# Optimization experiments

Hardware: AMD Instinct MI355X
Metric: run time of the kernel (lower is better)

Reference implementation:

```python
import jax, jax.numpy as jnp
import numpy as np

DECAY = 0.99
EPS = 1e-5
BETA = 0.25

def _l2norm(v, axis=-1):
    # F.normalize: x / max(||x||, 1e-12)
    n = jnp.sqrt(jnp.sum(v * v, axis=axis, keepdims=True))
    return v / jnp.maximum(n, 1e-12)

def setup_inputs() -> dict:
    key = jax.random.key(0)
    k0, k1, k2, k3 = jax.random.split(key, 4)
    B, C, H, W, E, K = 8, 256, 64, 64, 32, 8192
    x = jax.random.normal(k0, (B, C, H, W), jnp.float32)
    Wq = jax.random.normal(k1, (E, C), jnp.float32) * 0.05  # 1x1 conv kernel
    bq = jnp.zeros((E,), jnp.float32)
    emb = jax.random.normal(k2, (K, E), jnp.float32)
    emb = _l2norm(emb, axis=1)  # matches F.normalize init in __init__
    ema_cluster_size = jnp.ones((K,), jnp.float32)
    ema_weight = emb  # consistent post-init EMA state
    return {"x": x, "Wq": Wq, "bq": bq, "embedding": emb,
            "ema_cluster_size": ema_cluster_size, "ema_weight": ema_weight}

def reference(x, Wq, bq, embedding, ema_cluster_size, ema_weight):
    B, C, H, W = x.shape
    E = Wq.shape[0]
    K = embedding.shape[0]
    # quant_conv: 1x1 conv == per-pixel linear
    z = jnp.einsum('bchw,ec->behw', x, Wq) + bq[None, :, None, None]  # [B,E,H,W]
    z_flat = z.transpose(0, 2, 3, 1).reshape(-1, E)  # [N,E]
    # get_idx(use_znorm=True): cosine similarity argmax (== argmin L2 on normalized)
    zn = _l2norm(z_flat, axis=1)
    en = _l2norm(embedding, axis=1)
    indices = jnp.argmax(zn @ en.T, axis=1)  # [N]
    # codebook gather (raw embedding, as in torch)
    z_q = embedding[indices].reshape(B, H, W, E).transpose(0, 3, 1, 2)  # [B,E,H,W]
    # EMA update (training path; scatter == one-hot.T @ z_flat / one-hot.sum)
    counts = jax.ops.segment_sum(jnp.ones((z_flat.shape[0],), z_flat.dtype), indices, num_segments=K)
    dw = jax.ops.segment_sum(z_flat, indices, num_segments=K)  # [K,E]
    new_cs = DECAY * ema_cluster_size + (1.0 - DECAY) * counts
    new_w = DECAY * ema_weight + (1.0 - DECAY) * dw
    n = jnp.sum(new_cs)
    cs_smoothed = (new_cs + EPS) / (n + K * EPS) * n
    new_embedding = new_w / cs_smoothed[:, None]
    # commitment loss + straight-through
    qloss = BETA * jnp.mean((jax.lax.stop_gradient(z_q) - z) ** 2)
    z_q_st = z + jax.lax.stop_gradient(z_q - z)
    return (z_q_st, indices.reshape(B, H, W), qloss, new_embedding, new_cs, new_w)
```

## Files before the change

kernel.cpp:

```cpp
#include <hip/hip_runtime.h>

#define B_ 8
#define C_ 256
#define HW_ 4096
#define E_ 32
#define K_ 8192
#define N_ 32768
#define NCHUNK 8
#define KC_ (K_ / NCHUNK)
#define NSTAGE (KC_ / 128)
#define KSEG 16
#define PIX 256

#define DECAY_ 0.99f
#define OMD_   0.01f
#define EPS_   1e-5f
#define BETA_  0.25f

#define O_ZQ   0
#define O_IDX  1048576
#define O_QL   1081344
#define O_NEMB 1081345
#define O_NCS  1343489
#define O_NW   1351681

#define WS_EH   0u
#define WS_EM   131072u
#define WS_Z    262144u
#define WS_PACK 1310720u
#define WS_PCS  1835008u
#define WS_QP   1835024u

typedef float f32x4 __attribute__((ext_vector_type(4)));
typedef short s16x8 __attribute__((ext_vector_type(8)));
typedef unsigned long long u64;

__device__ __forceinline__ unsigned short f2bf(float f) {
    unsigned u = __float_as_uint(f);
    u = u + 0x7fffu + ((u >> 16) & 1u);
    return (unsigned short)(u >> 16);
}
__device__ __forceinline__ float bf2f(unsigned short h) {
    return __uint_as_float(((unsigned)h) << 16);
}
__device__ __forceinline__ unsigned ford(float f) {
    unsigned u = __float_as_uint(f);
    return (u & 0x80000000u) ? ~u : (u | 0x80000000u);
}
__device__ __forceinline__ int imax(int a, int b) { return a > b ? a : b; }
__device__ __forceinline__ int imin(int a, int b) { return a < b ? a : b; }

__device__ __forceinline__ void gload_lds16(const void* g, void* l) {
    __builtin_amdgcn_global_load_lds(
        (const __attribute__((address_space(1))) unsigned int*)g,
        (__attribute__((address_space(3))) unsigned int*)l, 16, 0, 0);
}

__global__ __launch_bounds__(512) void k_pre(const float* __restrict__ emb,
                                             const float* __restrict__ cs,
                                             uint4* __restrict__ eh16,
                                             uint4* __restrict__ em16,
                                             float* __restrict__ part_cs,
                                             const float* __restrict__ x,
                                             const float* __restrict__ Wq,
                                             const float* __restrict__ bq,
                                             float* __restrict__ zout) {
    __shared__ float wqt[C_ * E_];
    __shared__ float red8[8];
    int tid = threadIdx.x;

    if (blockIdx.x < 16) {
        int k = blockIdx.x * 512 + tid;
        const float4* r = (const float4*)(emb + (size_t)k * E_);
        float v[E_];
        float ss = 0.f;
#pragma unroll
        for (int i = 0; i < 8; i++) {
            float4 t = r[i];
            v[i*4+0] = t.x; v[i*4+1] = t.y; v[i*4+2] = t.z; v[i*4+3] = t.w;
            ss += t.x*t.x + t.y*t.y + t.z*t.z + t.w*t.w;
        }
        float inv = 1.0f / fmaxf(sqrtf(ss), 1e-12f);
        unsigned short h1a[E_], h2a[E_];
#pragma unroll
        for (int e = 0; e < E_; e++) {
            float en = v[e] * inv;
            unsigned short h1 = f2bf(en);
            float r1 = en - bf2f(h1);
            h1a[e] = h1; h2a[e] = f2bf(r1);
        }
        int t = k >> 4, c15 = k & 15;
#pragma unroll
        for (int i = 0; i < 4; i++) {
            eh16[t * 64 + i * 16 + c15] = ((uint4*)h1a)[i];
            em16[t * 64 + i * 16 + c15] = ((uint4*)h2a)[i];
        }

        float cv = cs[blockIdx.x * 512 + tid];
#pragma unroll
        for (int off = 32; off > 0; off >>= 1) cv += __shfl_down(cv, off);
        int lane = tid & 63, wid = tid >> 6;
        if (lane == 0) red8[wid] = cv;
        __syncthreads();
        if (tid == 0) {
            float s = 0.f;
#pragma unroll
            for (int i = 0; i < 8; i++) s += red8[i];
            part_cs[blockIdx.x] = s;
        }
        return;
    }

    int zb = blockIdx.x - 16;
#pragma unroll
    for (int i = 0; i < 16; i++) {
        int g = i * 512 + tid;
        int e = g >> 8;
        int c = g & 255;
        wqt[c * E_ + e] = Wq[g];
    }
    __syncthreads();
    int lp = tid & 63, eg = tid >> 6;
    int n0 = zb * 64 + lp;
    int b  = n0 >> 12, hw = n0 & (HW_ - 1);
    const float* xp = x + (size_t)b * C_ * HW_ + hw;
    float a0 = 0.f, a1 = 0.f, a2 = 0.f, a3 = 0.f;
#pragma unroll 8
    for (int c = 0; c < C_; c++) {
        float xv = xp[(size_t)c * HW_];
        float4 wv = *(const float4*)(wqt + c * E_ + eg * 4);
        a0 += xv * wv.x; a1 += xv * wv.y; a2 += xv * wv.z; a3 += xv * wv.w;
    }
    *(float4*)(zout + (size_t)n0 * E_ + eg * 4) =
        make_float4(a0 + bq[eg*4+0], a1 + bq[eg*4+1],
                    a2 + bq[eg*4+2], a3 + bq[eg*4+3]);
}

__global__ __launch_bounds__(512) void k_score_mfma(const float* __restrict__ zws,
                                                    const char* __restrict__ ehb,
                                                    const char* __restrict__ emb_b,
                                                    int2* __restrict__ pk2) {
    __shared__ __align__(16) char smem[32768];

    int tid  = threadIdx.x;
    int lane = tid & 63;
    int w    = tid >> 6;
    int chunk = blockIdx.y;

    s16x8 a1A, a2A, a1B, a2B;
    {
        int plocA = w * 32 + (lane & 15);
        int e0    = (lane >> 4) * 8;
#pragma unroll
        for (int s = 0; s < 2; s++) {
            int n0 = blockIdx.x * PIX + plocA + s * 16;
            const float4* zp = (const float4*)(zws + (size_t)n0 * E_ + e0);
            float4 z0 = zp[0], z1 = zp[1];
            float zz[8] = {z0.x, z0.y, z0.z, z0.w, z1.x, z1.y, z1.z, z1.w};
            s16x8 h1v, h2v;
#pragma unroll
            for (int j = 0; j < 8; j++) {
                float zv = zz[j] * 134217728.0f;
                unsigned short h1 = f2bf(zv);
                float r1 = zv - bf2f(h1);
                h1v[j] = (short)h1; h2v[j] = (short)f2bf(r1);
            }
            if (s == 0) { a1A = h1v; a2A = h2v; }
            else        { a1B = h1v; a2B = h2v; }
        }
    }

    const char* srcp[2];
#pragma unroll
    for (int i = 0; i < 2; i++) {
        int d = i * 512 + tid;
        int pl = d >> 9, dd = d & 511;
        srcp[i] = (pl ? emb_b : ehb) + (size_t)chunk * (KC_ * 64) + dd * 16;
    }

#pragma unroll
    for (int i = 0; i < 2; i++)
        gload_lds16(srcp[i], smem + (i * 512 + tid) * 16);
    __syncthreads();

    int rbase = 8191 - chunk * KC_ - (lane & 15);
    int bqA1[4], bqA2[4], bqB1[4], bqB2[4];
#pragma unroll
    for (int j = 0; j < 4; j++) {
        bqA1[j] = (int)0x80000000; bqA2[j] = (int)0x80000000;
        bqB1[j] = (int)0x80000000; bqB2[j] = (int)0x80000000;
    }
    f32x4 zero4 = {0.f, 0.f, 0.f, 0.f};

    for (int st = 0; st < NSTAGE; st++) {
        if (st + 1 < NSTAGE) {
            char* dst = smem + ((st + 1) & 1) * 16384;
#pragma unroll
            for (int i = 0; i < 2; i++)
                gload_lds16(srcp[i] + (size_t)(st + 1) * 8192, dst + (i * 512 + tid) * 16);
        }
        const char* cur = smem + (st & 1) * 16384;
        int rst = rbase - st * 128;

#pragma unroll
        for (int g = 0; g < 2; g++) {
            int ct = g * 4;
            s16x8 b1[4], b2[4];
#pragma unroll
            for (int q = 0; q < 4; q++) {
                b1[q] = ((const s16x8*)(cur +        (ct + q) * 1024))[lane];
                b2[q] = ((const s16x8*)(cur + 8192 + (ct + q) * 1024))[lane];
            }
            int r0 = rst - ct * 16;
            {
                f32x4 acc[4];
#pragma unroll
                for (int q = 0; q < 4; q++)
                    acc[q] = __builtin_amdgcn_mfma_f32_16x16x32_bf16(a1A, b1[q], zero4, 0, 0, 0);
#pragma unroll
                for (int q = 0; q < 4; q++)
                    acc[q] = __builtin_amdgcn_mfma_f32_16x16x32_bf16(a1A, b2[q], acc[q], 0, 0, 0);
#pragma unroll
                for (int q = 0; q < 4; q++)
                    acc[q] = __builtin_amdgcn_mfma_f32_16x16x32_bf16(a2A, b1[q], acc[q], 0, 0, 0);
#pragma unroll
                for (int j = 0; j < 4; j++) {
                    int v0 = ((int)acc[0][j] & (int)0xFFFFE000) | r0;
                    int v1 = ((int)acc[1][j] & (int)0xFFFFE000) | (r0 - 16);
                    int v2 = ((int)acc[2][j] & (int)0xFFFFE000) | (r0 - 32);
                    int v3 = ((int)acc[3][j] & (int)0xFFFFE000) | (r0 - 48);
                    int hi = imax(imax(v0, v1), imax(v2, v3));
                    int m  = imin(bqA1[j], hi);
                    bqA1[j] = imax(bqA1[j], hi);
                    bqA2[j] = imax(bqA2[j], m);
                }
            }
            {
                f32x4 acc[4];
#pragma unroll
                for (int q = 0; q < 4; q++)
                    acc[q] = __builtin_amdgcn_mfma_f32_16x16x32_bf16(a1B, b1[q], zero4, 0, 0, 0);
#pragma unroll
                for (int q = 0; q < 4; q++)
                    acc[q] = __builtin_amdgcn_mfma_f32_16x16x32_bf16(a1B, b2[q], acc[q], 0, 0, 0);
#pragma unroll
                for (int q = 0; q < 4; q++)
                    acc[q] = __builtin_amdgcn_mfma_f32_16x16x32_bf16(a2B, b1[q], acc[q], 0, 0, 0);
#pragma unroll
                for (int j = 0; j < 4; j++) {
                    int v0 = ((int)acc[0][j] & (int)0xFFFFE000) | r0;
                    int v1 = ((int)acc[1][j] & (int)0xFFFFE000) | (r0 - 16);
                    int v2 = ((int)acc[2][j] & (int)0xFFFFE000) | (r0 - 32);
                    int v3 = ((int)acc[3][j] & (int)0xFFFFE000) | (r0 - 48);
                    int hi = imax(imax(v0, v1), imax(v2, v3));
                    int m  = imin(bqB1[j], hi);
                    bqB1[j] = imax(bqB1[j], hi);
                    bqB2[j] = imax(bqB2[j], m);
                }
            }
        }
        __syncthreads();
    }

#pragma unroll
    for (int off = 1; off < 16; off <<= 1) {
#pragma unroll
        for (int j = 0; j < 4; j++) {
            int o1 = __shfl_xor(bqA1[j], off, 64);
            int o2 = __shfl_xor(bqA2[j], off, 64);
            int m  = imin(bqA1[j], o1);
            bqA1[j] = imax(bqA1[j], o1);
            bqA2[j] = imax(imax(bqA2[j], o2), m);
            int p1 = __shfl_xor(bqB1[j], off, 64);
            int p2 = __shfl_xor(bqB2[j], off, 64);
            int n  = imin(bqB1[j], p1);
            bqB1[j] = imax(bqB1[j], p1);
            bqB2[j] = imax(imax(bqB2[j], p2), n);
        }
    }
    if ((lane & 15) == 0) {
        int rowbase = blockIdx.x * PIX + w * 32 + (lane >> 4) * 4;
#pragma unroll
        for (int j = 0; j < 4; j++) {
            pk2[(size_t)chunk * N_ + rowbase + j]      = make_int2(bqA1[j], bqA2[j]);
            pk2[(size_t)chunk * N_ + rowbase + 16 + j] = make_int2(bqB1[j], bqB2[j]);
        }
    }
}

__device__ __forceinline__ float rescore(const float* __restrict__ emb, int k,
                                         const float* zrow) {
    const float4* r = (const float4*)(emb + (size_t)k * E_);
    float4 v[8];
    float ss = 0.f;
#pragma unroll
    for (int i = 0; i < 8; i++) {
        v[i] = r[i];
        ss += v[i].x * v[i].x + v[i].y * v[i].y + v[i].z * v[i].z + v[i].w * v[i].w;
    }
    float inv = 1.0f / fmaxf(sqrtf(ss), 1e-12f);
    const float4* zp = (const float4*)zrow;
    float sx = 0.f, sy = 0.f, sz = 0.f, sw = 0.f;
#pragma unroll
    for (int i = 0; i < 8; i++) {
        float4 e4 = make_float4(v[i].x * inv, v[i].y * inv, v[i].z * inv, v[i].w * inv);
        float4 zr = zp[i];
        sx += zr.x * e4.x; sy += zr.y * e4.y;
        sz += zr.z * e4.z; sw += zr.w * e4.w;
    }
    return (sx + sy) + (sz + sw);
}

__global__ __launch_bounds__(256) void k_scatter(const float* __restrict__ zws,
                                                 const int2* __restrict__ pk2,
                                                 const float* __restrict__ emb,
                                                 float* __restrict__ out_zq,
                                                 float* __restrict__ out_idx,
                                                 float* __restrict__ qpart) {
    __shared__ float zbuf[32 * E_];
    __shared__ int   idxs_s[32];
    __shared__ float red[4];
    int tid = threadIdx.x;

    const float4* zsrc = (const float4*)(zws + (size_t)blockIdx.x * 32 * E_);
    ((float4*)zbuf)[tid] = zsrc[tid];
    __syncthreads();

    {
        int p = tid >> 3, c8 = tid & 7;
        int nn = blockIdx.x * 32 + p;
        int2 c2 = pk2[(size_t)c8 * N_ + nn];
        u64 pkd = 0;
#pragma unroll
        for (int t = 0; t < 2; t++) {
            int raw = t ? c2.y : c2.x;
            int k = 8191 - (raw & 0x1fff);
            k = k < 0 ? 0 : (k > K_ - 1 ? K_ - 1 : k);
            float s = rescore(emb, k, zbuf + p * E_);
            u64 pk = ((u64)ford(s) << 32) | (unsigned)(K_ - 1 - k);
            pkd = pkd > pk ? pkd : pk;
        }
        u64 o = __shfl_xor(pkd, 1, 64); pkd = pkd > o ? pkd : o;
        o = __shfl_xor(pkd, 2, 64);     pkd = pkd > o ? pkd : o;
        o = __shfl_xor(pkd, 4, 64);     pkd = pkd > o ? pkd : o;
        if (c8 == 0) {
            int bi = K_ - 1 - (int)(unsigned)(pkd & 0xffffffffu);
            idxs_s[p] = bi;
            out_idx[nn] = (float)bi;
        }
    }
    __syncthreads();

    int lp = tid & 31, eg = tid >> 5;
    int n  = blockIdx.x * 32 + lp;
    int b  = n >> 12, hw = n & (HW_ - 1);
    int idx = idxs_s[lp];
    float4 e4 = *(const float4*)(emb + (size_t)idx * E_ + eg * 4);
    float* o = out_zq + (size_t)b * E_ * HW_ + (size_t)(eg * 4) * HW_ + hw;

    float z0 = zbuf[lp * E_ + eg * 4 + 0];
    float z1 = zbuf[lp * E_ + eg * 4 + 1];
    float z2 = zbuf[lp * E_ + eg * 4 + 2];
    float z3 = zbuf[lp * E_ + eg * 4 + 3];
    o[0]                 = e4.x;
    o[(size_t)1 * HW_]   = e4.y;
    o[(size_t)2 * HW_]   = e4.z;
    o[(size_t)3 * HW_]   = e4.w;
    float d0 = e4.x - z0, d1 = e4.y - z1, d2 = e4.z - z2, d3 = e4.w - z3;
    float sq = d0*d0 + d1*d1 + d2*d2 + d3*d3;

#pragma unroll
    for (int off = 32; off > 0; off >>= 1) sq += __shfl_down(sq, off);
    int lane = tid & 63, wid = tid >> 6;
    if (lane == 0) red[wid] = sq;
    __syncthreads();
    if (tid == 0) qpart[blockIdx.x] = red[0] + red[1] + red[2] + red[3];
}

__global__ __launch_bounds__(256) void k_dwfinal(const float* __restrict__ zws,
                                                 const float* __restrict__ idxf,
                                                 const float* __restrict__ cs,
                                                 const float* __restrict__ ew,
                                                 const float* __restrict__ part_cs,
                                                 const float* __restrict__ qpart,
                                                 float* __restrict__ out_nw,
                                                 float* __restrict__ out_nemb,
                                                 float* __restrict__ out_ncs,
                                                 float* __restrict__ out_ql) {
    __shared__ float acc[KSEG * E_];
    __shared__ int   cnt_s[KSEG];
    __shared__ int   plist[2048];
    __shared__ int   lcnt;
    __shared__ float nsum_s;
    int tid = threadIdx.x;
    int kbase = blockIdx.x * KSEG;

#pragma unroll
    for (int i = 0; i < KSEG * E_ / 256; i++) acc[tid + i * 256] = 0.f;
    if (tid < KSEG) cnt_s[tid] = 0;
    if (tid == 0) lcnt = 0;
    __syncthreads();

    const float4* idx4 = (const float4*)idxf;
    for (int tile = 0; tile < N_ / 2048; ++tile) {
        int pbase = tile * 2048 + tid * 8;
        float4 f0 = idx4[tile * 512 + tid * 2];
        float4 f1 = idx4[tile * 512 + tid * 2 + 1];
        float fs[8] = {f0.x, f0.y, f0.z, f0.w, f1.x, f1.y, f1.z, f1.w};
#pragma unroll
        for (int s = 0; s < 8; s++) {
            unsigned d = (unsigned)((int)fs[s] - kbase);
            if (d < (unsigned)KSEG) {
                int pos = atomicAdd(&lcnt, 1);
                plist[pos] = ((pbase + s) << 5) | (int)d;
                atomicAdd(cnt_s + (int)d, 1);
            }
        }
        __syncthreads();
        int cnt = lcnt;
        int e = tid & 31;
        for (int m = tid >> 5; m < cnt; m += 8) {
            int pk = plist[m];
            int nn = pk >> 5;
            float zv = zws[(size_t)nn * E_ + e];
            atomicAdd(acc + (pk & 31) * E_ + e, zv);
        }
        __syncthreads();
        if (tid == 0) lcnt = 0;
        __syncthreads();
    }

    if (tid < 64) {
        float s = (tid < 16) ? part_cs[tid] : 0.f;
        s += __shfl_down(s, 8);
        s += __shfl_down(s, 4);
        s += __shfl_down(s, 2);
        s += __shfl_down(s, 1);
        if (tid == 0) nsum_s = DECAY_ * s + OMD_ * (float)N_;
    }
    __syncthreads();
    float nsum = nsum_s;

#pragma unroll
    for (int i = 0; i < KSEG * E_ / 256; i++) {
        int local = tid + i * 256;
        int kl = local >> 5, c = local & 31;
        int k = kbase + kl;
        float v = DECAY_ * ew[(size_t)k * E_ + c] + OMD_ * acc[local];
        out_nw[(size_t)k * E_ + c] = v;
        float csk = DECAY_ * cs[k] + OMD_ * (float)cnt_s[kl];
        float denom = (csk + EPS_) / (nsum + (float)K_ * EPS_) * nsum;
        out_nemb[(size_t)k * E_ + c] = v / denom;
        if (c == 0) out_ncs[k] = csk;
    }

    if (blockIdx.x == 0 && tid < 64) {
        float s = 0.f;
#pragma unroll
        for (int i = 0; i < 16; i++) s += qpart[tid + i * 64];
#pragma unroll
        for (int off = 32; off > 0; off >>= 1) s += __shfl_down(s, off);
        if (tid == 0) out_ql[0] = BETA_ * s / (float)(B_ * E_ * HW_);
    }
}

extern "C" void kernel_launch(void* const* d_in, const int* in_sizes, int n_in,
                              void* d_out, int out_size, void* d_ws, size_t ws_size,
                              hipStream_t stream) {
    const float* x   = (const float*)d_in[0];
    const float* Wq  = (const float*)d_in[1];
    const float* bq  = (const float*)d_in[2];
    const float* emb = (const float*)d_in[3];
    const float* cs  = (const float*)d_in[4];
    const float* ew  = (const float*)d_in[5];
    float* out = (float*)d_out;
    float* ws  = (float*)d_ws;

    k_pre<<<16 + N_ / 64, 512, 0, stream>>>(emb, cs,
        (uint4*)(ws + WS_EH), (uint4*)(ws + WS_EM), ws + WS_PCS,
        x, Wq, bq, ws + WS_Z);
    k_score_mfma<<<dim3(N_ / PIX, NCHUNK), 512, 0, stream>>>(ws + WS_Z,
        (const char*)(ws + WS_EH), (const char*)(ws + WS_EM),
        (int2*)(ws + WS_PACK));
    k_scatter<<<N_ / 32, 256, 0, stream>>>(ws + WS_Z,
        (const int2*)(ws + WS_PACK), emb,
        out + O_ZQ, out + O_IDX, ws + WS_QP);
    k_dwfinal<<<K_ / KSEG, 256, 0, stream>>>(ws + WS_Z, out + O_IDX, cs, ew,
                                             ws + WS_PCS, ws + WS_QP,
                                             out + O_NW, out + O_NEMB,
                                             out + O_NCS, out + O_QL);
}
```

Before: 188.1 us.

## Precompute codebook inverse norms, halve k_pre block size, double KSEG

```diff
diff --git a/kernel.cpp b/kernel.cpp
--- a/kernel.cpp
+++ b/kernel.cpp
@@ -9,7 +9,7 @@
 #define NCHUNK 8
 #define KC_ (K_ / NCHUNK)
 #define NSTAGE (KC_ / 128)
-#define KSEG 16
+#define KSEG 32
 #define PIX 256
 
 #define DECAY_ 0.99f
@@ -29,7 +29,8 @@
 #define WS_Z    262144u
 #define WS_PACK 1310720u
 #define WS_PCS  1835008u
-#define WS_QP   1835024u
+#define WS_QP   1835040u
+#define WS_INV  1836064u
 
 typedef float f32x4 __attribute__((ext_vector_type(4)));
 typedef short s16x8 __attribute__((ext_vector_type(8)));
@@ -56,21 +57,22 @@
         (__attribute__((address_space(3))) unsigned int*)l, 16, 0, 0);
 }
 
-__global__ __launch_bounds__(512) void k_pre(const float* __restrict__ emb,
+__global__ __launch_bounds__(256) void k_pre(const float* __restrict__ emb,
                                              const float* __restrict__ cs,
                                              uint4* __restrict__ eh16,
                                              uint4* __restrict__ em16,
                                              float* __restrict__ part_cs,
+                                             float* __restrict__ invn,
                                              const float* __restrict__ x,
                                              const float* __restrict__ Wq,
                                              const float* __restrict__ bq,
                                              float* __restrict__ zout) {
     __shared__ float wqt[C_ * E_];
-    __shared__ float red8[8];
+    __shared__ float red4[4];
     int tid = threadIdx.x;
 
-    if (blockIdx.x < 16) {
-        int k = blockIdx.x * 512 + tid;
+    if (blockIdx.x < 32) {
+        int k = blockIdx.x * 256 + tid;
         const float4* r = (const float4*)(emb + (size_t)k * E_);
         float v[E_];
         float ss = 0.f;
@@ -81,6 +83,7 @@
             ss += t.x*t.x + t.y*t.y + t.z*t.z + t.w*t.w;
         }
         float inv = 1.0f / fmaxf(sqrtf(ss), 1e-12f);
+        invn[k] = inv;
         unsigned short h1a[E_], h2a[E_];
 #pragma unroll
         for (int e = 0; e < E_; e++) {
@@ -96,44 +99,45 @@
             em16[t * 64 + i * 16 + c15] = ((uint4*)h2a)[i];
         }
 
-        float cv = cs[blockIdx.x * 512 + tid];
+        float cv = cs[blockIdx.x * 256 + tid];
 #pragma unroll
         for (int off = 32; off > 0; off >>= 1) cv += __shfl_down(cv, off);
         int lane = tid & 63, wid = tid >> 6;
-        if (lane == 0) red8[wid] = cv;
+        if (lane == 0) red4[wid] = cv;
         __syncthreads();
-        if (tid == 0) {
-            float s = 0.f;
-#pragma unroll
-            for (int i = 0; i < 8; i++) s += red8[i];
-            part_cs[blockIdx.x] = s;
-        }
+        if (tid == 0) part_cs[blockIdx.x] = red4[0] + red4[1] + red4[2] + red4[3];
         return;
     }
 
-    int zb = blockIdx.x - 16;
-#pragma unroll
-    for (int i = 0; i < 16; i++) {
-        int g = i * 512 + tid;
+    int zb = blockIdx.x - 32;
+#pragma unroll
+    for (int i = 0; i < 32; i++) {
+        int g = i * 256 + tid;
         int e = g >> 8;
         int c = g & 255;
         wqt[c * E_ + e] = Wq[g];
     }
     __syncthreads();
-    int lp = tid & 63, eg = tid >> 6;
+    int lp = tid & 31, eg = tid >> 5;
     int n0 = zb * 64 + lp;
     int b  = n0 >> 12, hw = n0 & (HW_ - 1);
     const float* xp = x + (size_t)b * C_ * HW_ + hw;
-    float a0 = 0.f, a1 = 0.f, a2 = 0.f, a3 = 0.f;
+    float a[8];
+#pragma unroll
+    for (int j = 0; j < 8; j++) a[j] = 0.f;
 #pragma unroll 8
     for (int c = 0; c < C_; c++) {
-        float xv = xp[(size_t)c * HW_];
+        float xa = xp[(size_t)c * HW_];
+        float xb = xp[(size_t)c * HW_ + 32];
         float4 wv = *(const float4*)(wqt + c * E_ + eg * 4);
-        a0 += xv * wv.x; a1 += xv * wv.y; a2 += xv * wv.z; a3 += xv * wv.w;
-    }
+        a[0] += xa * wv.x; a[1] += xa * wv.y; a[2] += xa * wv.z; a[3] += xa * wv.w;
+        a[4] += xb * wv.x; a[5] += xb * wv.y; a[6] += xb * wv.z; a[7] += xb * wv.w;
+    }
+    float bq0 = bq[eg*4+0], bq1v = bq[eg*4+1], bq2v = bq[eg*4+2], bq3 = bq[eg*4+3];
     *(float4*)(zout + (size_t)n0 * E_ + eg * 4) =
-        make_float4(a0 + bq[eg*4+0], a1 + bq[eg*4+1],
-                    a2 + bq[eg*4+2], a3 + bq[eg*4+3]);
+        make_float4(a[0]+bq0, a[1]+bq1v, a[2]+bq2v, a[3]+bq3);
+    *(float4*)(zout + (size_t)(n0 + 32) * E_ + eg * 4) =
+        make_float4(a[4]+bq0, a[5]+bq1v, a[6]+bq2v, a[7]+bq3);
 }
 
 __global__ __launch_bounds__(512) void k_score_mfma(const float* __restrict__ zws,
@@ -288,32 +292,26 @@
     }
 }
 
-__device__ __forceinline__ float rescore(const float* __restrict__ emb, int k,
+__device__ __forceinline__ float rescore(const float* __restrict__ emb,
+                                         const float* __restrict__ invn, int k,
                                          const float* zrow) {
     const float4* r = (const float4*)(emb + (size_t)k * E_);
-    float4 v[8];
-    float ss = 0.f;
-#pragma unroll
-    for (int i = 0; i < 8; i++) {
-        v[i] = r[i];
-        ss += v[i].x * v[i].x + v[i].y * v[i].y + v[i].z * v[i].z + v[i].w * v[i].w;
-    }
-    float inv = 1.0f / fmaxf(sqrtf(ss), 1e-12f);
     const float4* zp = (const float4*)zrow;
     float sx = 0.f, sy = 0.f, sz = 0.f, sw = 0.f;
 #pragma unroll
     for (int i = 0; i < 8; i++) {
-        float4 e4 = make_float4(v[i].x * inv, v[i].y * inv, v[i].z * inv, v[i].w * inv);
+        float4 e4 = r[i];
         float4 zr = zp[i];
         sx += zr.x * e4.x; sy += zr.y * e4.y;
         sz += zr.z * e4.z; sw += zr.w * e4.w;
     }
-    return (sx + sy) + (sz + sw);
+    return ((sx + sy) + (sz + sw)) * invn[k];
 }
 
 __global__ __launch_bounds__(256) void k_scatter(const float* __restrict__ zws,
                                                  const int2* __restrict__ pk2,
                                                  const float* __restrict__ emb,
+                                                 const float* __restrict__ invn,
                                                  float* __restrict__ out_zq,
                                                  float* __restrict__ out_idx,
                                                  float* __restrict__ qpart) {
@@ -336,7 +334,7 @@
             int raw = t ? c2.y : c2.x;
             int k = 8191 - (raw & 0x1fff);
             k = k < 0 ? 0 : (k > K_ - 1 ? K_ - 1 : k);
-            float s = rescore(emb, k, zbuf + p * E_);
+            float s = rescore(emb, invn, k, zbuf + p * E_);
             u64 pk = ((u64)ford(s) << 32) | (unsigned)(K_ - 1 - k);
             pkd = pkd > pk ? pkd : pk;
         }
@@ -431,7 +429,8 @@
     }
 
     if (tid < 64) {
-        float s = (tid < 16) ? part_cs[tid] : 0.f;
+        float s = (tid < 32) ? part_cs[tid] : 0.f;
+        s += __shfl_down(s, 16);
         s += __shfl_down(s, 8);
         s += __shfl_down(s, 4);
         s += __shfl_down(s, 2);
@@ -476,14 +475,14 @@
     float* out = (float*)d_out;
     float* ws  = (float*)d_ws;
 
-    k_pre<<<16 + N_ / 64, 512, 0, stream>>>(emb, cs,
-        (uint4*)(ws + WS_EH), (uint4*)(ws + WS_EM), ws + WS_PCS,
+    k_pre<<<32 + N_ / 64, 256, 0, stream>>>(emb, cs,
+        (uint4*)(ws + WS_EH), (uint4*)(ws + WS_EM), ws + WS_PCS, ws + WS_INV,
         x, Wq, bq, ws + WS_Z);
     k_score_mfma<<<dim3(N_ / PIX, NCHUNK), 512, 0, stream>>>(ws + WS_Z,
         (const char*)(ws + WS_EH), (const char*)(ws + WS_EM),
         (int2*)(ws + WS_PACK));
     k_scatter<<<N_ / 32, 256, 0, stream>>>(ws + WS_Z,
-        (const int2*)(ws + WS_PACK), emb,
+        (const int2*)(ws + WS_PACK), emb, ws + WS_INV,
         out + O_ZQ, out + O_IDX, ws + WS_QP);
     k_dwfinal<<<K_ / KSEG, 256, 0, stream>>>(ws + WS_Z, out + O_IDX, cs, ew,
                                              ws + WS_PCS, ws + WS_QP,
```

Measured after the change: 196.7 us. 1.05x slower.
